# Performance work log

Hardware: AMD Instinct MI355X
Metric: run time of the kernel (lower is better)

## Reference

```python
import jax, jax.numpy as jnp
import numpy as np


def _conv1x1(x, W, b):
    # x: (B,C,H,W), W: (O,C), b: (O,)
    return jnp.einsum('bchw,oc->bohw', x, W) + b[None, :, None, None]


def _maxpool2(x):
    B, C, H, W = x.shape
    return x.reshape(B, C, H // 2, 2, W // 2, 2).max(axis=(3, 5))


def setup_inputs() -> dict:
    key = jax.random.key(0)
    ks = jax.random.split(key, 6)
    B, C, H, W = 8, 1024, 64, 64
    DI, DO = 512, 1024
    std = 0.01  # matches nn.init.normal_(std=0.01)
    return {
        'x': jax.random.normal(ks[0], (B, C, H, W), dtype=jnp.float32),
        'W_theta': std * jax.random.normal(ks[1], (DI, C), dtype=jnp.float32),
        'b_theta': jnp.zeros((DI,), jnp.float32),
        'W_phi': std * jax.random.normal(ks[2], (DI, C), dtype=jnp.float32),
        'b_phi': jnp.zeros((DI,), jnp.float32),
        'W_g': std * jax.random.normal(ks[3], (DI, C), dtype=jnp.float32),
        'b_g': jnp.zeros((DI,), jnp.float32),
        'W_out': std * jax.random.normal(ks[4], (DO, DI), dtype=jnp.float32),
        'b_out': jnp.zeros((DO,), jnp.float32),
    }


def reference(x, W_theta, b_theta, W_phi, b_phi, W_g, b_g, W_out, b_out):
    B, C, H, W = x.shape
    di = W_theta.shape[0]
    scale = di ** (-0.5)
    # queries from full-res map: (B, di, N) with N = H*W
    theta = _conv1x1(x, W_theta, b_theta).reshape(B, di, H * W)
    # keys/values from 2x2-maxpooled map: (B, di, M), M = (H/2)*(W/2)
    px = _maxpool2(x)
    phi = _conv1x1(px, W_phi, b_phi).reshape(B, di, -1)
    g = _conv1x1(px, W_g, b_g).reshape(B, di, -1)
    # attention: (B, N, M)
    logits = jnp.einsum('bdn,bdm->bnm', theta, phi) * scale
    p = jax.nn.softmax(logits, axis=-1)
    # aggregate values: (B, di, N) -> (B, di, H, W)
    t = jnp.einsum('bdm,bnm->bdn', g, p).reshape(B, di, H, W)
    y = _conv1x1(t, W_out, b_out)
    return y + x
```

## Files before the change

kernel.cpp:

```cpp
#include <hip/hip_runtime.h>
#include <hip/hip_bf16.h>
#include <stdint.h>

typedef __bf16 bf16;
typedef __bf16 bf16x8 __attribute__((ext_vector_type(8)));
typedef __bf16 bf16x4 __attribute__((ext_vector_type(4)));
typedef float f32x4 __attribute__((ext_vector_type(4)));

#define GLOAD_LDS16(gptr, lptr)                                                        \
  __builtin_amdgcn_global_load_lds((const __attribute__((address_space(1))) void*)(gptr), \
                                   (__attribute__((address_space(3))) void*)(lptr), 16, 0, 0)

__global__ __launch_bounds__(256) void cast_f2b(const float* __restrict__ in,
                                                bf16* __restrict__ out, int n) {
  int i = (blockIdx.x * 256 + threadIdx.x) * 4;
  if (i >= n) return;
  const float4 v = *(const float4*)(in + i);
  bf16x4 o;
  o[0] = (bf16)v.x; o[1] = (bf16)v.y; o[2] = (bf16)v.z; o[3] = (bf16)v.w;
  *(bf16x4*)(out + i) = o;
}

__global__ __launch_bounds__(256) void prep_kernel(const float* __restrict__ x,
                                                   bf16* __restrict__ xbT,
                                                   bf16* __restrict__ pxT) {
  const int b = blockIdx.y;
  x   += (size_t)b * 1024 * 4096;
  xbT += (size_t)b * 4096 * 1024;
  pxT += (size_t)b * 1024 * 1024;
  const int bid = blockIdx.x;
  const int h0 = bid & 31, ct = bid >> 5;
  const int tid = threadIdx.x;
  __shared__ float tile[32][129];
  const float* xs = x + (size_t)(ct * 32) * 4096 + h0 * 128;
#pragma unroll
  for (int e = 0; e < 16; ++e) {
    int idx = e * 256 + tid;
    int c = idx >> 7, n = idx & 127;
    tile[c][n] = xs[(size_t)c * 4096 + n];
  }
  __syncthreads();
  bf16* xo = xbT + (size_t)(h0 * 128) * 1024 + ct * 32;
#pragma unroll
  for (int e = 0; e < 16; ++e) {
    int idx = e * 256 + tid;
    int n = idx >> 5, c = idx & 31;
    xo[(size_t)n * 1024 + c] = (bf16)tile[c][n];
  }
  bf16* po = pxT + (size_t)(h0 * 32) * 1024 + ct * 32;
#pragma unroll
  for (int e = 0; e < 4; ++e) {
    int idx = e * 256 + tid;
    int m = idx >> 5, c = idx & 31;
    float v = fmaxf(fmaxf(tile[c][2 * m], tile[c][2 * m + 1]),
                    fmaxf(tile[c][64 + 2 * m], tile[c][64 + 2 * m + 1]));
    po[(size_t)m * 1024 + c] = (bf16)v;
  }
}

__global__ __launch_bounds__(256) void rowsum_k(const bf16* __restrict__ P,
                                                float* __restrict__ rs) {
  const int row = blockIdx.x * 4 + (threadIdx.x >> 6);
  const int lane = threadIdx.x & 63;
  const bf16* Pr = P + (size_t)row * 1024;
  bf16x8 v0 = *(const bf16x8*)(Pr + lane * 16);
  bf16x8 v1 = *(const bf16x8*)(Pr + lane * 16 + 8);
  float s = 0.f;
#pragma unroll
  for (int e = 0; e < 8; ++e) s += (float)v0[e] + (float)v1[e];
#pragma unroll
  for (int o = 32; o > 0; o >>= 1) s += __shfl_xor(s, o);
  if (lane == 0) rs[row] = s;
}

template <int EPI>
__global__ __launch_bounds__(256) void gemm_bt(
    const bf16* __restrict__ A, long long sA, int lda,
    const bf16* __restrict__ B, long long sB, int ldb,
    void* __restrict__ Cv, long long sC, int ldc, int K,
    const float* __restrict__ bias,
    const float* __restrict__ resid, long long sResid, float scale) {
  const int z = blockIdx.z;
  A += (size_t)z * sA;
  B += (size_t)z * sB;
  const int tid = threadIdx.x;
  const int w = tid >> 6, lane = tid & 63;
  const int r16 = lane & 15, q4 = lane >> 4;
  const long long tileM = (long long)blockIdx.x * 128;
  const long long tileN = (long long)blockIdx.y * 128;

  __shared__ bf16 As[2][128 * 32];
  __shared__ bf16 Bs[2][128 * 32];

  f32x4 acc[4][4] = {};

  const int srow = tid >> 2;
  const int soff = (tid & 3) * 16;
  const char* Ag0 = (const char*)A + ((size_t)(tileM + srow) * lda) * 2 + soff;
  const char* Bg0 = (const char*)B + ((size_t)(tileN + srow) * ldb) * 2 + soff;
  const size_t arow64 = (size_t)64 * lda * 2;
  const size_t brow64 = (size_t)64 * ldb * 2;

  auto stage = [&](int buf, int k0) {
    const char* a = Ag0 + (size_t)k0 * 2;
    const char* b = Bg0 + (size_t)k0 * 2;
    bf16* al = &As[buf][w * 512];
    bf16* bl = &Bs[buf][w * 512];
    GLOAD_LDS16(a, al);
    GLOAD_LDS16(a + arow64, al + 2048);
    GLOAD_LDS16(b, bl);
    GLOAD_LDS16(b + brow64, bl + 2048);
  };

  const int wr = (w >> 1) * 64, wc = (w & 1) * 64;
  const int nt = K >> 5;
  stage(0, 0);
  __syncthreads();
  int cur = 0;
  for (int t = 0; t < nt; ++t) {
    if (t + 1 < nt) stage(cur ^ 1, (t + 1) * 32);
    bf16x8 af[4], bfv[4];
#pragma unroll
    for (int f = 0; f < 4; ++f) {
      af[f]  = *(const bf16x8*)&As[cur][(wr + f * 16 + r16) * 32 + q4 * 8];
      bfv[f] = *(const bf16x8*)&Bs[cur][(wc + f * 16 + r16) * 32 + q4 * 8];
    }
#pragma unroll
    for (int i = 0; i < 4; ++i)
#pragma unroll
      for (int j = 0; j < 4; ++j)
        acc[i][j] = __builtin_amdgcn_mfma_f32_16x16x32_bf16(af[i], bfv[j], acc[i][j], 0, 0, 0);
    __syncthreads();
    cur ^= 1;
  }

  if constexpr (EPI == 4) {
    float* C = (float*)Cv + (size_t)z * sC;
#pragma unroll
    for (int i = 0; i < 4; ++i) {
      const int row0 = (int)tileM + wr + i * 16 + q4 * 4;
#pragma unroll
      for (int j = 0; j < 4; ++j) {
        const int col = (int)tileN + wc + j * 16 + r16;
#pragma unroll
        for (int r = 0; r < 4; ++r) {
          float v = acc[i][j][r];
          v += bias[row0 + r];
          v += resid[(size_t)z * sResid + (size_t)(row0 + r) * ldc + col];
          C[(size_t)(row0 + r) * ldc + col] = v;
        }
      }
    }
  } else if constexpr (EPI == 5) {
    bf16* C = (bf16*)Cv + (size_t)z * sC;
#pragma unroll
    for (int i = 0; i < 4; ++i) {
      const int row0 = (int)tileM + wr + i * 16 + q4 * 4;
#pragma unroll
      for (int j = 0; j < 4; ++j) {
        const int col = (int)tileN + wc + j * 16 + r16;
#pragma unroll
        for (int r = 0; r < 4; ++r)
          C[(size_t)(row0 + r) * ldc + col] = (bf16)__expf(acc[i][j][r]);
      }
    }
  } else if constexpr (EPI == 7) {
    bf16* C = (bf16*)Cv + (size_t)z * sC;
    const float* rsp = bias + (size_t)z * 4096;
#pragma unroll
    for (int i = 0; i < 4; ++i) {
      const int row0 = (int)tileM + wr + i * 16 + q4 * 4;
      float inv[4];
#pragma unroll
      for (int r = 0; r < 4; ++r) inv[r] = 1.0f / rsp[row0 + r];
#pragma unroll
      for (int j = 0; j < 4; ++j) {
        const int col = (int)tileN + wc + j * 16 + r16;
#pragma unroll
        for (int r = 0; r < 4; ++r)
          C[(size_t)(row0 + r) * ldc + col] = (bf16)(acc[i][j][r] * inv[r]);
      }
    }
  } else {
    bf16* C = (bf16*)Cv + (size_t)z * sC;
#pragma unroll
    for (int i = 0; i < 4; ++i) {
      const int row0 = (int)tileM + wr + i * 16 + q4 * 4;
#pragma unroll
      for (int j = 0; j < 4; ++j) {
        const int col = (int)tileN + wc + j * 16 + r16;
        float badd = 0.f;
        if constexpr (EPI == 1) badd = bias[col];
#pragma unroll
        for (int r = 0; r < 4; ++r) {
          float v = acc[i][j][r];
          if constexpr (EPI == 1) v = (v + badd) * scale;
          if constexpr (EPI == 2) v += bias[row0 + r];
          C[(size_t)(row0 + r) * ldc + col] = (bf16)v;
        }
      }
    }
  }
}

extern "C" void kernel_launch(void* const* d_in, const int* in_sizes, int n_in,
                              void* d_out, int out_size, void* d_ws, size_t ws_size,
                              hipStream_t stream) {
  const float* x  = (const float*)d_in[0];
  const float* Wt = (const float*)d_in[1];
  const float* bt = (const float*)d_in[2];
  const float* Wp = (const float*)d_in[3];
  const float* bp = (const float*)d_in[4];
  const float* Wg = (const float*)d_in[5];
  const float* bg = (const float*)d_in[6];
  const float* Wo = (const float*)d_in[7];
  const float* bo = (const float*)d_in[8];
  float* out = (float*)d_out;

  const size_t MB = 1024ull * 1024ull;
  char* ws = (char*)d_ws;
  bf16* WtB = (bf16*)(ws + 0 * MB);
  bf16* WpB = (bf16*)(ws + 1 * MB);
  bf16* WgB = (bf16*)(ws + 2 * MB);
  bf16* WoB = (bf16*)(ws + 3 * MB);

  cast_f2b<<<512, 256, 0, stream>>>(Wt, WtB, 512 * 1024);
  cast_f2b<<<512, 256, 0, stream>>>(Wp, WpB, 512 * 1024);
  cast_f2b<<<512, 256, 0, stream>>>(Wg, WgB, 512 * 1024);
  cast_f2b<<<512, 256, 0, stream>>>(Wo, WoB, 1024 * 512);

  const float SCALE = 0.044194173824159216f;

  auto run_g6 = [&](int nb, int b0, bf16* tT) {
    gemm_bt<4><<<dim3(8, 32, nb), 256, 0, stream>>>(WoB, 0, 512, tT, 4096ll * 512, 512,
                                                    out + (size_t)b0 * 1024 * 4096,
                                                    1024ll * 4096, 4096, 512,
                                                    bo, x + (size_t)b0 * 1024 * 4096,
                                                    1024ll * 4096, 1.f);
  };

  if (ws_size >= 164 * MB) {
    bf16* pxT    = (bf16*)(ws + 4 * MB);
    bf16* phiT   = (bf16*)(ws + 20 * MB);
    bf16* g      = (bf16*)(ws + 28 * MB);
    bf16* thetaT = (bf16*)(ws + 36 * MB);
    bf16* tT     = (bf16*)(ws + 68 * MB);
    bf16* xbT    = (bf16*)(ws + 100 * MB);
    bf16*  Pt   = (bf16*)d_out;
    float* rsum = (float*)((char*)d_out + 80 * MB);

    prep_kernel<<<dim3(1024, 8), 256, 0, stream>>>(x, xbT, pxT);
    gemm_bt<1><<<dim3(32, 4, 8), 256, 0, stream>>>(xbT, 4096ll * 1024, 1024, WtB, 0, 1024,
                                                   thetaT, 4096ll * 512, 512, 1024,
                                                   bt, nullptr, 0, SCALE);
    gemm_bt<1><<<dim3(8, 4, 8), 256, 0, stream>>>(pxT, 1024ll * 1024, 1024, WpB, 0, 1024,
                                                  phiT, 1024ll * 512, 512, 1024,
                                                  bp, nullptr, 0, 1.f);
    gemm_bt<2><<<dim3(4, 8, 8), 256, 0, stream>>>(WgB, 0, 1024, pxT, 1024ll * 1024, 1024,
                                                  g, 512ll * 1024, 1024, 1024,
                                                  bg, nullptr, 0, 1.f);
    gemm_bt<5><<<dim3(32, 8, 8), 256, 0, stream>>>(thetaT, 4096ll * 512, 512,
                                                   phiT, 1024ll * 512, 512,
                                                   Pt, 4096ll * 1024, 1024, 512,
                                                   nullptr, nullptr, 0, 1.f);
    rowsum_k<<<8192, 256, 0, stream>>>(Pt, rsum);
    gemm_bt<7><<<dim3(32, 4, 8), 256, 0, stream>>>(Pt, 4096ll * 1024, 1024,
                                                   g, 512ll * 1024, 1024,
                                                   tT, 4096ll * 512, 512, 1024,
                                                   rsum, nullptr, 0, 1.f);
    run_g6(8, 0, tT);
  } else if (ws_size >= 108 * MB) {
    bf16* pxT    = (bf16*)(ws + 4 * MB);
    bf16* phiT   = (bf16*)(ws + 20 * MB);
    bf16* g      = (bf16*)(ws + 28 * MB);
    bf16* thetaT = (bf16*)(ws + 36 * MB);
    bf16* tT     = (bf16*)(ws + 68 * MB);
    bf16* xbT    = (bf16*)(ws + 100 * MB);
    float* rsum = (float*)((char*)d_out + 80 * MB);
    for (int b = 0; b < 8; ++b) {
      prep_kernel<<<dim3(1024, 1), 256, 0, stream>>>(x + (size_t)b * 1024 * 4096, xbT,
                                                     pxT + (size_t)b * 1024 * 1024);
      gemm_bt<1><<<dim3(32, 4, 1), 256, 0, stream>>>(xbT, 0, 1024, WtB, 0, 1024,
                                                     thetaT + (size_t)b * 4096 * 512, 0, 512,
                                                     1024, bt, nullptr, 0, SCALE);
    }
    gemm_bt<1><<<dim3(8, 4, 8), 256, 0, stream>>>(pxT, 1024ll * 1024, 1024, WpB, 0, 1024,
                                                  phiT, 1024ll * 512, 512, 1024,
                                                  bp, nullptr, 0, 1.f);
    gemm_bt<2><<<dim3(4, 8, 8), 256, 0, stream>>>(WgB, 0, 1024, pxT, 1024ll * 1024, 1024,
                                                  g, 512ll * 1024, 1024, 1024,
                                                  bg, nullptr, 0, 1.f);
    for (int b = 0; b < 8; ++b) {
      bf16* Ptb = (bf16*)d_out + (size_t)b * 4096 * 1024;
      gemm_bt<5><<<dim3(32, 8, 1), 256, 0, stream>>>(thetaT + (size_t)b * 4096 * 512, 0, 512,
                                                     phiT + (size_t)b * 1024 * 512, 0, 512,
                                                     Ptb, 0, 1024, 512,
                                                     nullptr, nullptr, 0, 1.f);
      rowsum_k<<<1024, 256, 0, stream>>>(Ptb, rsum + (size_t)b * 4096);
      gemm_bt<7><<<dim3(32, 4, 1), 256, 0, stream>>>(Ptb, 0, 1024,
                                                     g + (size_t)b * 512 * 1024, 0, 1024,
                                                     tT + (size_t)b * 4096 * 512, 0, 512, 1024,
                                                     rsum + (size_t)b * 4096, nullptr, 0, 1.f);
    }
    run_g6(8, 0, tT);
  } else {
    float* rsum  = (float*)(ws + 4 * MB);
    bf16* pxT    = (bf16*)(ws + 5 * MB);
    bf16* phiT   = (bf16*)(ws + 7 * MB);
    bf16* g      = (bf16*)(ws + 8 * MB);
    bf16* thetaT = (bf16*)(ws + 9 * MB);
    bf16* tT     = (bf16*)(ws + 13 * MB);
    bf16* Pt     = (bf16*)(ws + 17 * MB);
    bf16* xbT    = (bf16*)(ws + 25 * MB);
    for (int b = 0; b < 8; ++b) {
      prep_kernel<<<dim3(1024, 1), 256, 0, stream>>>(x + (size_t)b * 1024 * 4096, xbT, pxT);
      gemm_bt<1><<<dim3(32, 4, 1), 256, 0, stream>>>(xbT, 0, 1024, WtB, 0, 1024,
                                                     thetaT, 0, 512, 1024,
                                                     bt, nullptr, 0, SCALE);
      gemm_bt<1><<<dim3(8, 4, 1), 256, 0, stream>>>(pxT, 0, 1024, WpB, 0, 1024,
                                                    phiT, 0, 512, 1024,
                                                    bp, nullptr, 0, 1.f);
      gemm_bt<2><<<dim3(4, 8, 1), 256, 0, stream>>>(WgB, 0, 1024, pxT, 0, 1024,
                                                    g, 0, 1024, 1024,
                                                    bg, nullptr, 0, 1.f);
      gemm_bt<5><<<dim3(32, 8, 1), 256, 0, stream>>>(thetaT, 0, 512, phiT, 0, 512,
                                                     Pt, 0, 1024, 512,
                                                     nullptr, nullptr, 0, 1.f);
      rowsum_k<<<1024, 256, 0, stream>>>(Pt, rsum);
      gemm_bt<7><<<dim3(32, 4, 1), 256, 0, stream>>>(Pt, 0, 1024, g, 0, 1024,
                                                     tT, 0, 512, 1024,
                                                     rsum, nullptr, 0, 1.f);
      run_g6(1, b, tT);
    }
  }
}
```

Measured before the change: 357.0 us.

## Add 256x256-tile GEMM with 4-stage LDS pipeline for large GEMMs

Introduces gemm256, a 512-thread kernel computing 256x256 output tiles with a 4-deep LDS ring buffer, XOR-swizzled LDS layout, explicit vmcnt waits, and setprio around MFMA bursts. The large GEMMs (theta projection, logits/exp, P·g, output projection with residual) are switched to it, while the small phi/g GEMMs keep the old kernel. The aim is more data reuse per tile and deeper load/compute overlap. The cost is one block per CU, 64 KB of LDS, and heavy register pressure from 32 accumulators per lane, which could lower occupancy or cause spills. The old kernel's epilogue is trimmed to the bias-only variants it still serves.

Result: faster. 322.9 us (-9.5%).

```diff
diff --git a/kernel.cpp b/kernel.cpp
--- a/kernel.cpp
+++ b/kernel.cpp
@@ -71,6 +71,158 @@
 #pragma unroll
   for (int o = 32; o > 0; o >>= 1) s += __shfl_xor(s, o);
   if (lane == 0) rs[row] = s;
+}
+
+template <int EPI>
+__global__ __launch_bounds__(512, 1) void gemm256(
+    const bf16* __restrict__ A, long long sA, int lda,
+    const bf16* __restrict__ B, long long sB, int ldb,
+    void* __restrict__ Cv, long long sC, int ldc, int K,
+    const float* __restrict__ bias,
+    const float* __restrict__ resid, long long sResid, float scale) {
+  const int z = blockIdx.z;
+  A += (size_t)z * sA;
+  B += (size_t)z * sB;
+  const int tid = threadIdx.x;
+  const int w = tid >> 6, lane = tid & 63;
+  const int r16 = lane & 15, q4 = lane >> 4;
+  const int wm = w >> 2, wn = w & 3;
+  const long long tileM = (long long)blockIdx.x * 256;
+  const long long tileN = (long long)blockIdx.y * 256;
+
+  __shared__ bf16 As[4][8192];
+  __shared__ bf16 Bs[4][8192];
+
+  f32x4 acc[8][4] = {};
+
+  const int srow = tid >> 2;
+  const int skb  = (tid & 3) ^ ((srow >> 1) & 3);
+  const char* Ag = (const char*)A + ((size_t)(tileM + srow) * lda + skb * 8) * 2;
+  const char* Bg = (const char*)B + ((size_t)(tileN + srow) * ldb + skb * 8) * 2;
+  const size_t a128 = (size_t)128 * lda * 2;
+  const size_t b128 = (size_t)128 * ldb * 2;
+
+  auto stA = [&](int T) {
+    bf16* d = &As[T & 3][w * 512];
+    const char* s = Ag + (size_t)T * 64;
+    GLOAD_LDS16(s, d);
+    GLOAD_LDS16(s + a128, d + 4096);
+  };
+  auto stB = [&](int T) {
+    bf16* d = &Bs[T & 3][w * 512];
+    const char* s = Bg + (size_t)T * 64;
+    GLOAD_LDS16(s, d);
+    GLOAD_LDS16(s + b128, d + 4096);
+  };
+
+  stA(0); stB(0); stA(1); stB(1);
+  const int NT = K >> 5;
+
+  for (int T = 0; T < NT; ++T) {
+    if (T + 2 < NT) stA(T + 2);
+    if (T + 2 < NT)      asm volatile("s_waitcnt vmcnt(6)" ::: "memory");
+    else if (T + 1 < NT) asm volatile("s_waitcnt vmcnt(4)" ::: "memory");
+    else                 asm volatile("s_waitcnt vmcnt(0)" ::: "memory");
+    __builtin_amdgcn_s_barrier();
+    asm volatile("" ::: "memory");
+
+    const char* Asl = (const char*)&As[T & 3][0];
+    const char* Bsl = (const char*)&Bs[T & 3][0];
+    bf16x8 bf_[4];
+#pragma unroll
+    for (int ni = 0; ni < 4; ++ni) {
+      const int row = wn * 64 + ni * 16 + r16;
+      bf_[ni] = *(const bf16x8*)(Bsl + row * 64 + ((q4 ^ ((row >> 1) & 3)) << 4));
+    }
+    bf16x8 af[4];
+#pragma unroll
+    for (int mi = 0; mi < 4; ++mi) {
+      const int row = wm * 128 + mi * 16 + r16;
+      af[mi] = *(const bf16x8*)(Asl + row * 64 + ((q4 ^ ((row >> 1) & 3)) << 4));
+    }
+    __builtin_amdgcn_s_setprio(1);
+#pragma unroll
+    for (int mi = 0; mi < 4; ++mi)
+#pragma unroll
+      for (int ni = 0; ni < 4; ++ni)
+        acc[mi][ni] = __builtin_amdgcn_mfma_f32_16x16x32_bf16(af[mi], bf_[ni], acc[mi][ni], 0, 0, 0);
+    __builtin_amdgcn_s_setprio(0);
+
+    if (T + 2 < NT) stB(T + 2);
+#pragma unroll
+    for (int mi = 0; mi < 4; ++mi) {
+      const int row = wm * 128 + 64 + mi * 16 + r16;
+      af[mi] = *(const bf16x8*)(Asl + row * 64 + ((q4 ^ ((row >> 1) & 3)) << 4));
+    }
+    __builtin_amdgcn_s_setprio(1);
+#pragma unroll
+    for (int mi = 0; mi < 4; ++mi)
+#pragma unroll
+      for (int ni = 0; ni < 4; ++ni)
+        acc[4 + mi][ni] = __builtin_amdgcn_mfma_f32_16x16x32_bf16(af[mi], bf_[ni], acc[4 + mi][ni], 0, 0, 0);
+    __builtin_amdgcn_s_setprio(0);
+  }
+
+  if constexpr (EPI == 4) {
+    float* C = (float*)Cv + (size_t)z * sC;
+    const float* rz = resid + (size_t)z * sResid;
+#pragma unroll
+    for (int a = 0; a < 8; ++a) {
+      const int row0 = (int)tileM + wm * 128 + a * 16 + q4 * 4;
+#pragma unroll
+      for (int ni = 0; ni < 4; ++ni) {
+        const int col = (int)tileN + wn * 64 + ni * 16 + r16;
+#pragma unroll
+        for (int r = 0; r < 4; ++r)
+          C[(size_t)(row0 + r) * ldc + col] =
+              acc[a][ni][r] + bias[row0 + r] + rz[(size_t)(row0 + r) * ldc + col];
+      }
+    }
+  } else if constexpr (EPI == 5) {
+    bf16* C = (bf16*)Cv + (size_t)z * sC;
+#pragma unroll
+    for (int a = 0; a < 8; ++a) {
+      const int row0 = (int)tileM + wm * 128 + a * 16 + q4 * 4;
+#pragma unroll
+      for (int ni = 0; ni < 4; ++ni) {
+        const int col = (int)tileN + wn * 64 + ni * 16 + r16;
+#pragma unroll
+        for (int r = 0; r < 4; ++r)
+          C[(size_t)(row0 + r) * ldc + col] = (bf16)__expf(acc[a][ni][r]);
+      }
+    }
+  } else if constexpr (EPI == 7) {
+    bf16* C = (bf16*)Cv + (size_t)z * sC;
+    const float* rsp = bias + (size_t)z * 4096;
+#pragma unroll
+    for (int a = 0; a < 8; ++a) {
+      const int row0 = (int)tileM + wm * 128 + a * 16 + q4 * 4;
+      float inv[4];
+#pragma unroll
+      for (int r = 0; r < 4; ++r) inv[r] = 1.0f / rsp[row0 + r];
+#pragma unroll
+      for (int ni = 0; ni < 4; ++ni) {
+        const int col = (int)tileN + wn * 64 + ni * 16 + r16;
+#pragma unroll
+        for (int r = 0; r < 4; ++r)
+          C[(size_t)(row0 + r) * ldc + col] = (bf16)(acc[a][ni][r] * inv[r]);
+      }
+    }
+  } else {
+    bf16* C = (bf16*)Cv + (size_t)z * sC;
+#pragma unroll
+    for (int a = 0; a < 8; ++a) {
+      const int row0 = (int)tileM + wm * 128 + a * 16 + q4 * 4;
+#pragma unroll
+      for (int ni = 0; ni < 4; ++ni) {
+        const int col = (int)tileN + wn * 64 + ni * 16 + r16;
+        const float badd = bias[col];
+#pragma unroll
+        for (int r = 0; r < 4; ++r)
+          C[(size_t)(row0 + r) * ldc + col] = (bf16)((acc[a][ni][r] + badd) * scale);
+      }
+    }
+  }
 }
 
 template <int EPI>
@@ -134,70 +286,21 @@
     cur ^= 1;
   }
 
-  if constexpr (EPI == 4) {
-    float* C = (float*)Cv + (size_t)z * sC;
-#pragma unroll
-    for (int i = 0; i < 4; ++i) {
-      const int row0 = (int)tileM + wr + i * 16 + q4 * 4;
-#pragma unroll
-      for (int j = 0; j < 4; ++j) {
-        const int col = (int)tileN + wc + j * 16 + r16;
-#pragma unroll
-        for (int r = 0; r < 4; ++r) {
-          float v = acc[i][j][r];
-          v += bias[row0 + r];
-          v += resid[(size_t)z * sResid + (size_t)(row0 + r) * ldc + col];
-          C[(size_t)(row0 + r) * ldc + col] = v;
-        }
-      }
-    }
-  } else if constexpr (EPI == 5) {
-    bf16* C = (bf16*)Cv + (size_t)z * sC;
-#pragma unroll
-    for (int i = 0; i < 4; ++i) {
-      const int row0 = (int)tileM + wr + i * 16 + q4 * 4;
-#pragma unroll
-      for (int j = 0; j < 4; ++j) {
-        const int col = (int)tileN + wc + j * 16 + r16;
-#pragma unroll
-        for (int r = 0; r < 4; ++r)
-          C[(size_t)(row0 + r) * ldc + col] = (bf16)__expf(acc[i][j][r]);
-      }
-    }
-  } else if constexpr (EPI == 7) {
-    bf16* C = (bf16*)Cv + (size_t)z * sC;
-    const float* rsp = bias + (size_t)z * 4096;
-#pragma unroll
-    for (int i = 0; i < 4; ++i) {
-      const int row0 = (int)tileM + wr + i * 16 + q4 * 4;
-      float inv[4];
-#pragma unroll
-      for (int r = 0; r < 4; ++r) inv[r] = 1.0f / rsp[row0 + r];
-#pragma unroll
-      for (int j = 0; j < 4; ++j) {
-        const int col = (int)tileN + wc + j * 16 + r16;
-#pragma unroll
-        for (int r = 0; r < 4; ++r)
-          C[(size_t)(row0 + r) * ldc + col] = (bf16)(acc[i][j][r] * inv[r]);
-      }
-    }
-  } else {
-    bf16* C = (bf16*)Cv + (size_t)z * sC;
-#pragma unroll
-    for (int i = 0; i < 4; ++i) {
-      const int row0 = (int)tileM + wr + i * 16 + q4 * 4;
-#pragma unroll
-      for (int j = 0; j < 4; ++j) {
-        const int col = (int)tileN + wc + j * 16 + r16;
-        float badd = 0.f;
-        if constexpr (EPI == 1) badd = bias[col];
-#pragma unroll
-        for (int r = 0; r < 4; ++r) {
-          float v = acc[i][j][r];
-          if constexpr (EPI == 1) v = (v + badd) * scale;
-          if constexpr (EPI == 2) v += bias[row0 + r];
-          C[(size_t)(row0 + r) * ldc + col] = (bf16)v;
-        }
+  bf16* C = (bf16*)Cv + (size_t)z * sC;
+#pragma unroll
+  for (int i = 0; i < 4; ++i) {
+    const int row0 = (int)tileM + wr + i * 16 + q4 * 4;
+#pragma unroll
+    for (int j = 0; j < 4; ++j) {
+      const int col = (int)tileN + wc + j * 16 + r16;
+      float badd = 0.f;
+      if constexpr (EPI == 1) badd = bias[col];
+#pragma unroll
+      for (int r = 0; r < 4; ++r) {
+        float v = acc[i][j][r];
+        if constexpr (EPI == 1) v = (v + badd) * scale;
+        if constexpr (EPI == 2) v += bias[row0 + r];
+        C[(size_t)(row0 + r) * ldc + col] = (bf16)v;
       }
     }
   }
@@ -232,7 +335,7 @@
   const float SCALE = 0.044194173824159216f;
 
   auto run_g6 = [&](int nb, int b0, bf16* tT) {
-    gemm_bt<4><<<dim3(8, 32, nb), 256, 0, stream>>>(WoB, 0, 512, tT, 4096ll * 512, 512,
+    gemm256<4><<<dim3(4, 16, nb), 512, 0, stream>>>(WoB, 0, 512, tT, 4096ll * 512, 512,
                                                     out + (size_t)b0 * 1024 * 4096,
                                                     1024ll * 4096, 4096, 512,
                                                     bo, x + (size_t)b0 * 1024 * 4096,
@@ -250,7 +353,7 @@
     float* rsum = (float*)((char*)d_out + 80 * MB);
 
     prep_kernel<<<dim3(1024, 8), 256, 0, stream>>>(x, xbT, pxT);
-    gemm_bt<1><<<dim3(32, 4, 8), 256, 0, stream>>>(xbT, 4096ll * 1024, 1024, WtB, 0, 1024,
+    gemm256<1><<<dim3(16, 2, 8), 512, 0, stream>>>(xbT, 4096ll * 1024, 1024, WtB, 0, 1024,
                                                    thetaT, 4096ll * 512, 512, 1024,
                                                    bt, nullptr, 0, SCALE);
     gemm_bt<1><<<dim3(8, 4, 8), 256, 0, stream>>>(pxT, 1024ll * 1024, 1024, WpB, 0, 1024,
@@ -259,12 +362,12 @@
     gemm_bt<2><<<dim3(4, 8, 8), 256, 0, stream>>>(WgB, 0, 1024, pxT, 1024ll * 1024, 1024,
                                                   g, 512ll * 1024, 1024, 1024,
                                                   bg, nullptr, 0, 1.f);
-    gemm_bt<5><<<dim3(32, 8, 8), 256, 0, stream>>>(thetaT, 4096ll * 512, 512,
+    gemm256<5><<<dim3(16, 4, 8), 512, 0, stream>>>(thetaT, 4096ll * 512, 512,
                                                    phiT, 1024ll * 512, 512,
                                                    Pt, 4096ll * 1024, 1024, 512,
                                                    nullptr, nullptr, 0, 1.f);
     rowsum_k<<<8192, 256, 0, stream>>>(Pt, rsum);
-    gemm_bt<7><<<dim3(32, 4, 8), 256, 0, stream>>>(Pt, 4096ll * 1024, 1024,
+    gemm256<7><<<dim3(16, 2, 8), 512, 0, stream>>>(Pt, 4096ll * 1024, 1024,
                                                    g, 512ll * 1024, 1024,
                                                    tT, 4096ll * 512, 512, 1024,
                                                    rsum, nullptr, 0, 1.f);
@@ -280,7 +383,7 @@
     for (int b = 0; b < 8; ++b) {
       prep_kernel<<<dim3(1024, 1), 256, 0, stream>>>(x + (size_t)b * 1024 * 4096, xbT,
                                                      pxT + (size_t)b * 1024 * 1024);
-      gemm_bt<1><<<dim3(32, 4, 1), 256, 0, stream>>>(xbT, 0, 1024, WtB, 0, 1024,
+      gemm256<1><<<dim3(16, 2, 1), 512, 0, stream>>>(xbT, 0, 1024, WtB, 0, 1024,
                                                      thetaT + (size_t)b * 4096 * 512, 0, 512,
                                                      1024, bt, nullptr, 0, SCALE);
     }
@@ -292,12 +395,12 @@
                                                   bg, nullptr, 0, 1.f);
     for (int b = 0; b < 8; ++b) {
       bf16* Ptb = (bf16*)d_out + (size_t)b * 4096 * 1024;
-      gemm_bt<5><<<dim3(32, 8, 1), 256, 0, stream>>>(thetaT + (size_t)b * 4096 * 512, 0, 512,
+      gemm256<5><<<dim3(16, 4, 1), 512, 0, stream>>>(thetaT + (size_t)b * 4096 * 512, 0, 512,
                                                      phiT + (size_t)b * 1024 * 512, 0, 512,
                                                      Ptb, 0, 1024, 512,
                                                      nullptr, nullptr, 0, 1.f);
       rowsum_k<<<1024, 256, 0, stream>>>(Ptb, rsum + (size_t)b * 4096);
-      gemm_bt<7><<<dim3(32, 4, 1), 256, 0, stream>>>(Ptb, 0, 1024,
+      gemm256<7><<<dim3(16, 2, 1), 512, 0, stream>>>(Ptb, 0, 1024,
                                                      g + (size_t)b * 512 * 1024, 0, 1024,
                                                      tT + (size_t)b * 4096 * 512, 0, 512, 1024,
                                                      rsum + (size_t)b * 4096, nullptr, 0, 1.f);
@@ -314,7 +417,7 @@
     bf16* xbT    = (bf16*)(ws + 25 * MB);
     for (int b = 0; b < 8; ++b) {
       prep_kernel<<<dim3(1024, 1), 256, 0, stream>>>(x + (size_t)b * 1024 * 4096, xbT, pxT);
-      gemm_bt<1><<<dim3(32, 4, 1), 256, 0, stream>>>(xbT, 0, 1024, WtB, 0, 1024,
+      gemm256<1><<<dim3(16, 2, 1), 512, 0, stream>>>(xbT, 0, 1024, WtB, 0, 1024,
                                                      thetaT, 0, 512, 1024,
                                                      bt, nullptr, 0, SCALE);
       gemm_bt<1><<<dim3(8, 4, 1), 256, 0, stream>>>(pxT, 0, 1024, WpB, 0, 1024,
@@ -323,11 +426,11 @@
       gemm_bt<2><<<dim3(4, 8, 1), 256, 0, stream>>>(WgB, 0, 1024, pxT, 0, 1024,
                                                     g, 0, 1024, 1024,
                                                     bg, nullptr, 0, 1.f);
-      gemm_bt<5><<<dim3(32, 8, 1), 256, 0, stream>>>(thetaT, 0, 512, phiT, 0, 512,
+      gemm256<5><<<dim3(16, 4, 1), 512, 0, stream>>>(thetaT, 0, 512, phiT, 0, 512,
                                                      Pt, 0, 1024, 512,
                                                      nullptr, nullptr, 0, 1.f);
       rowsum_k<<<1024, 256, 0, stream>>>(Pt, rsum);
-      gemm_bt<7><<<dim3(32, 4, 1), 256, 0, stream>>>(Pt, 0, 1024, g, 0, 1024,
+      gemm256<7><<<dim3(16, 2, 1), 512, 0, stream>>>(Pt, 0, 1024, g, 0, 1024,
                                                      tT, 0, 512, 1024,
                                                      rsum, nullptr, 0, 1.f);
       run_g6(1, b, tT);
```
